# Kernel optimization log

Measured on AMD Instinct MI355X. Metric: run time of the kernel, lower is better.

Reference implementation:

```python
import jax, jax.numpy as jnp
import numpy as np

V, E, H, T, B = 10004, 96, 670, 20, 256


def setup_inputs() -> dict:
    key = jax.random.key(0)
    ks = iter(jax.random.split(key, 48))
    def p(*shape):
        return jax.random.normal(next(ks), shape, jnp.float32) * 0.05
    emb = p(V, E).at[0].set(0.0)  # padding_idx=0 row zeroed
    return dict(
        x=jax.random.randint(next(ks), (B, T), 0, V, jnp.int32),
        emb=emb,
        g_wi=p(4 * H, E), g_wh=p(4 * H, H), g_bi=p(4 * H), g_bh=p(4 * H),
        l_wi=p(4 * H, E), l_wh=p(4 * H, H), l_bi=p(4 * H), l_bh=p(4 * H),
        gl1_w=p(E, H), gl1_b=p(E), ll1_w=p(E, H), ll1_b=p(E),
        gl2_w=p(V, E), gl2_b=p(V), ll2_w=p(V, E), ll2_b=p(V),
        p1_w=p(500, E + 2 * H), p1_b=p(500),
        p2_w=p(250, 500), p2_b=p(250),
        p3_w=p(100, 250), p3_b=p(100),
        p4_w=p(50, 100), p4_b=p(50),
        pe_w=p(2, 50), pe_b=p(2),
        q1_w=p(75, 192), q1_b=p(75),
        q2_w=p(30, 75), q2_b=p(30),
        q2e_w=p(2, 30), q2e_b=p(2),
        q3_w=p(10, 30), q3_b=p(10),
        q3e_w=p(2, 10), q3e_b=p(2),
    )


def _lstm(x, h, c, wi, wh, bi, bh):
    # torch.nn.LSTMCell gate order: i, f, g, o
    g = x @ wi.T + bi + h @ wh.T + bh
    i, f, gg, o = jnp.split(g, 4, axis=-1)
    c = jax.nn.sigmoid(f) * c + jax.nn.sigmoid(i) * jnp.tanh(gg)
    h = jax.nn.sigmoid(o) * jnp.tanh(c)
    return h, c


def reference(x, emb, g_wi, g_wh, g_bi, g_bh, l_wi, l_wh, l_bi, l_bh,
              gl1_w, gl1_b, ll1_w, ll1_b, gl2_w, gl2_b, ll2_w, ll2_b,
              p1_w, p1_b, p2_w, p2_b, p3_w, p3_b, p4_w, p4_b, pe_w, pe_b,
              q1_w, q1_b, q2_w, q2_b, q2e_w, q2e_b, q3_w, q3_b, q3e_w, q3e_b):
    relu = jax.nn.relu
    embs = emb[x]                      # [B,T,E]
    Bb, Tt = x.shape
    Hh = g_wh.shape[1]
    z0 = jnp.zeros((Bb, Hh), embs.dtype)

    def step(carry, e_t):
        gh, gc, lh, lc = carry
        gh, gc = _lstm(e_t, gh, gc, g_wi, g_wh, g_bi, g_bh)
        lh, lc = _lstm(e_t, lh, lc, l_wi, l_wh, l_bi, l_bh)
        h = relu(jnp.concatenate([e_t, gh, lh], 1) @ p1_w.T + p1_b)
        h = relu(h @ p2_w.T + p2_b)
        h = relu(h @ p3_w.T + p3_b)
        h = relu(h @ p4_w.T + p4_b)
        prob = jax.nn.softmax(h @ pe_w.T + pe_b, axis=1)  # [B,2]
        # bmm([B,1,2],[B,2,H]) with tilde=[local, global]
        ghm = prob[:, 0:1] * lh + prob[:, 1:2] * gh
        gcm = prob[:, 0:1] * lc + prob[:, 1:2] * gc
        return (ghm, gcm, lh, lc), (ghm, prob)

    _, (hs, probs) = jax.lax.scan(step, (z0, z0, z0, z0), jnp.swapaxes(embs, 0, 1))
    hidden_states = jnp.swapaxes(hs, 0, 1)    # [B,T,H]
    probs_loop = jnp.swapaxes(probs, 0, 1)    # [B,T,2]

    global_x = hidden_states @ gl1_w.T + gl1_b  # [B,T,E]
    local_x = hidden_states @ ll1_w.T + ll1_b   # [B,T,E]
    sf = jnp.concatenate([global_x, local_x], -1)  # [B,T,192]
    h = relu(sf @ q1_w.T + q1_b)
    h = relu(h @ q2_w.T + q2_b)
    y = relu(h @ q2e_w.T + q2e_b)               # p1 logits [B,T,2]
    h2 = relu(h @ q3_w.T + q3_b)
    zz = relu(h2 @ q3e_w.T + q3e_b)             # p2 logits [B,T,2]

    p1s = jax.nn.softmax(y, axis=2)
    ph = jnp.broadcast_to(probs_loop[:, :, None, :], (Bb, Tt, Tt, 2))  # repeat(1,1,T,1)
    ph = jnp.concatenate([ph, p1s[:, None, :, :]], axis=1)
    xm = p1s[:, :, 0:1] * global_x + p1s[:, :, 1:2] * local_x
    gl = xm @ gl2_w.T + gl2_b                   # [B,T,V]
    ll = xm @ ll2_w.T + ll2_b
    p2s = jax.nn.softmax(zz, axis=2)
    ph = jnp.concatenate([ph, p2s[:, None, :, :]], axis=1)  # [B,T+2,T,2]
    logits = gl * p2s[:, :, 0:1] + ll * p2s[:, :, 1:2]
    return jnp.transpose(logits, (0, 2, 1)), ph
```

## Files before the change

kernel.cpp:

```cpp
#include <hip/hip_runtime.h>

#define DI __device__ __forceinline__

typedef unsigned short u16;
typedef unsigned int u32;
typedef __bf16 bf16x8 __attribute__((ext_vector_type(8)));
typedef float f32x4 __attribute__((ext_vector_type(4)));
typedef u32 u32x4 __attribute__((ext_vector_type(4)));

static constexpr int B = 256, Tn = 20, En = 96, Hn = 670, Vn = 10004;
static constexpr int HP = 672;
static constexpr int NBLK = 336;
static constexpr int GT = NBLK * 256;

DI float bf2f(u16 u) { union { u32 i; float f; } v; v.i = ((u32)u) << 16; return v.f; }
DI u16 f2bf(float f) {
    u32 u = __float_as_uint(f);
    u32 r = (u + 0x7FFFu + ((u >> 16) & 1u)) >> 16;
    return (u16)r;
}
DI float sigm(float x) { return 1.f / (1.f + __expf(-x)); }
DI float tanha(float x) {
    x = fminf(fmaxf(x, -15.f), 15.f);
    float e = __expf(2.f * x);
    return (e - 1.f) / (e + 1.f);
}
DI bf16x8 frag(const u16* p) { return *(const bf16x8*)p; }
DI f32x4 mfma16(bf16x8 a, bf16x8 b, f32x4 c) {
    return __builtin_amdgcn_mfma_f32_16x16x32_bf16(a, b, c, 0, 0, 0);
}
DI u16 ldw(const u16* src, long long i, int f) {
    return f ? f2bf(((const float*)src)[i]) : src[i];
}
DI float ldf(const u16* src, long long i, int f) {
    return f ? ((const float*)src)[i] : bf2f(src[i]);
}

DI u32x4 ldg16(const void* p) {
    u32x4 v;
    asm volatile("global_load_dwordx4 %0, %1, off sc0 sc1\n\ts_waitcnt vmcnt(0)"
                 : "=v"(v) : "v"(p));
    return v;
}
DI void ldg4f(const float* p0, const float* p1, const float* p2, const float* p3,
              float& a, float& b, float& c, float& d) {
    asm volatile("global_load_dword %0, %4, off sc0 sc1\n\t"
                 "global_load_dword %1, %5, off sc0 sc1\n\t"
                 "global_load_dword %2, %6, off sc0 sc1\n\t"
                 "global_load_dword %3, %7, off sc0 sc1\n\t"
                 "s_waitcnt vmcnt(0)"
                 : "=&v"(a), "=&v"(b), "=&v"(c), "=&v"(d)
                 : "v"(p0), "v"(p1), "v"(p2), "v"(p3));
}
DI u32 ldgu32(const u32* p) {
    u32 v;
    asm volatile("global_load_dword %0, %1, off sc0 sc1\n\ts_waitcnt vmcnt(0)"
                 : "=v"(v) : "v"(p));
    return v;
}
DI void stg32(float* p, float v) {
    asm volatile("global_store_dword %0, %1, off sc0 sc1" :: "v"(p), "v"(v) : "memory");
}
DI void stgu32(u32* p, u32 v) {
    asm volatile("global_store_dword %0, %1, off sc0 sc1" :: "v"(p), "v"(v) : "memory");
}
DI void stg16(u16* p, u16 v) {
    asm volatile("global_store_short %0, %1, off sc0 sc1" :: "v"(p), "v"((u32)v) : "memory");
}

struct Ptrs {
    const int* x;
    const u16 *emb, *g_wi, *g_wh, *g_bi, *g_bh, *l_wi, *l_wh, *l_bi, *l_bh;
    const u16 *gl1_w, *gl1_b, *ll1_w, *ll1_b, *gl2_w, *gl2_b, *ll2_w, *ll2_b;
    const u16 *p1_w, *p1_b, *p2_w, *p2_b, *p3_w, *p3_b, *p4_w, *p4_b, *pe_w, *pe_b;
    const u16 *q1_w, *q1_b, *q2_w, *q2_b, *q2e_w, *q2e_b, *q3_w, *q3_b, *q3e_w, *q3e_b;
    unsigned *bar;
    int  *flagp;
    u16 *embs;
    u16 *WgCat;
    u16 *P1W;
    u16 *W1C;
    u16 *W2C;
    float *BSUM;
    u16 *hs;
    u16 *hcat;
    u16 *uw;
    float *ghf, *gcf, *lhf, *lc2, *gcm;
    float *L1out;
    float *sf;
    float *p2sbuf;
    u16 *n_p1b, *n_p2w, *n_p2b, *n_p3w, *n_p3b, *n_p4w, *n_p4b, *n_pew, *n_peb;
    u16 *n_gl1b, *n_ll1b, *n_gl2b, *n_ll2b;
    u16 *n_q1w, *n_q1b, *n_q2w, *n_q2b, *n_q2ew, *n_q2eb, *n_q3w, *n_q3b, *n_q3ew, *n_q3eb;
    u16 *out0, *out1;
    float *out0f, *out1f;
};

template<bool HEAVY>
DI void gbar(unsigned* bar, int bid, int tid, unsigned gen) {
    __syncthreads();
    if (tid == 0) {
        if (HEAVY) __threadfence();
        else asm volatile("s_waitcnt vmcnt(0)" ::: "memory");
        stgu32(&bar[32 + bid * 16], gen);
    }
    if (bid == 0) {
        for (int i = tid; i < NBLK; i += 256) {
            while ((int)(ldgu32(&bar[32 + i * 16]) - gen) < 0)
                __builtin_amdgcn_s_sleep(4);
        }
        __syncthreads();
        if (tid == 0) stgu32(&bar[0], gen);
    } else if (tid == 0) {
        while ((int)(ldgu32(&bar[0]) - gen) < 0)
            __builtin_amdgcn_s_sleep(8);
    }
    __syncthreads();
    if (HEAVY) {
        if (tid == 0) __threadfence();
        __syncthreads();
    }
}

__global__ __launch_bounds__(256) void k_detect(Ptrs p) {
    int tid = threadIdx.x;
    for (int i = tid; i < 8192; i += 256) p.bar[i] = 0u;
    if (tid < 64) {
        u32 d = ((const u32*)p.g_bi)[tid];
        u16 lo = (u16)(d & 0xffffu);
        int e = (lo >> 7) & 0xff;
        unsigned long long m = __ballot(e >= 127);
        if (tid == 0) p.flagp[0] = (m != 0ull) ? 1 : 0;
    }
}

struct SMg { u16 Al[32 * 72]; u16 Wl[128 * 72]; float bs[128]; };
struct SMm { u16 Al[32 * 72]; u16 Wl[32 * 72]; };
struct SMr { float l1[500]; float h2s[250]; float h3s[100]; float h4s[52]; float pr[4]; };
struct SMs { u16 Al[64 * 40]; u16 Wl[64 * 40]; };
struct SMq {
    float sfl[3840];
    float h1[20][80]; float h2[20][32]; float h3[20][12];
    float yv[20][2]; float zv[20][2]; float p1s[20][2]; float p2sl[20][2];
};
union alignas(16) SMem { SMg g; SMm m; SMr r; SMs s; SMq q; };

DI void norm_phase(const Ptrs& p, int gtid, int f) {
    const u16* srcs[23] = {p.p1_b, p.p2_w, p.p2_b, p.p3_w, p.p3_b, p.p4_w, p.p4_b,
                           p.pe_w, p.pe_b, p.gl1_b, p.ll1_b, p.gl2_b, p.ll2_b,
                           p.q1_w, p.q1_b, p.q2_w, p.q2_b, p.q2e_w, p.q2e_b,
                           p.q3_w, p.q3_b, p.q3e_w, p.q3e_b};
    u16* dsts[23] = {p.n_p1b, p.n_p2w, p.n_p2b, p.n_p3w, p.n_p3b, p.n_p4w, p.n_p4b,
                     p.n_pew, p.n_peb, p.n_gl1b, p.n_ll1b, p.n_gl2b, p.n_ll2b,
                     p.n_q1w, p.n_q1b, p.n_q2w, p.n_q2b, p.n_q2ew, p.n_q2eb,
                     p.n_q3w, p.n_q3b, p.n_q3ew, p.n_q3eb};
    const int ns[23] = {500, 125000, 250, 25000, 100, 5000, 50, 100, 2, 96, 96, 10004, 10004,
                        14400, 75, 2250, 30, 60, 2, 300, 10, 20, 2};
    for (int i0 = gtid; i0 < 193351; i0 += GT) {
        int i = i0;
        #pragma unroll 1
        for (int s = 0; s < 23; ++s) {
            if (i < ns[s]) { dsts[s][i] = ldw(srcs[s], i, f); break; }
            i -= ns[s];
        }
    }
}

DI void prep_one(const Ptrs& p, int i, int f) {
    if (i < 491520) {
        int r = i / 96, j = i % 96;
        int t = r >> 8, b = r & 255;
        int idx = p.x[b * Tn + t];
        p.embs[r * 96 + j] = ldw(p.emb, (long long)idx * 96 + j, f);
        return;
    }
    i -= 491520;
    if (i < 2 * 2680 * 768) {
        int z = i / (2680 * 768);
        int rem = i - z * (2680 * 768);
        int col = rem / 768, k = rem % 768;
        const u16* wi = z ? p.l_wi : p.g_wi;
        const u16* wh = z ? p.l_wh : p.g_wh;
        u16 v = 0;
        if (k < 96) v = ldw(wi, col * 96 + k, f);
        else { int j = k - 96; if (j < 670) v = ldw(wh, col * 670 + j, f); }
        p.WgCat[i] = v;
        return;
    }
    i -= 2 * 2680 * 768;
    if (i < 512 * 1472) {
        int col = i / 1472, k = i % 1472;
        u16 v = 0;
        if (col < 500) {
            if (k < 96) v = ldw(p.p1_w, col * 1436 + k, f);
            else if (k < 768) { int j = k - 96;  if (j < 670) v = ldw(p.p1_w, col * 1436 + 96 + j, f); }
            else              { int j = k - 768; if (j < 670) v = ldw(p.p1_w, col * 1436 + 766 + j, f); }
        }
        p.P1W[i] = v;
        return;
    }
    i -= 512 * 1472;
    if (i < 192 * 672) {
        int o = i / 672, h = i % 672;
        u16 v = 0;
        if (h < 670) v = (o < 96) ? ldw(p.gl1_w, o * 670 + h, f) : ldw(p.ll1_w, (o - 96) * 670 + h, f);
        p.W1C[i] = v;
        return;
    }
    i -= 192 * 672;
    if (i < 10112 * 192) {
        int v_ = i / 192, k = i % 192;
        u16 v = 0;
        if (v_ < Vn) v = (k < 96) ? ldw(p.gl2_w, v_ * 96 + k, f) : ldw(p.ll2_w, v_ * 96 + (k - 96), f);
        p.W2C[i] = v;
        return;
    }
    i -= 10112 * 192;
    if (i < 2 * 2680) {
        int z = i / 2680, col = i % 2680;
        const u16* bi = z ? p.l_bi : p.g_bi;
        const u16* bh = z ? p.l_bh : p.g_bh;
        p.BSUM[i] = ldf(bi, col, f) + ldf(bh, col, f);
    }
}

DI void gates_tile(const Ptrs& p, int t, int tau, int tid, SMg& S) {
    const int z = tau / 168;
    const int rem = tau - z * 168;
    const int jt = rem % 21, mt = rem / 21;
    const int row0 = mt * 32, j0 = jt * 32;
    const int lane = tid & 63, wv = tid >> 6;

    __syncthreads();
    if (tid < 128) {
        int gate = tid >> 5, jj = tid & 31, j = j0 + jj;
        S.bs[tid] = (j < Hn) ? p.BSUM[z * 2680 + gate * Hn + j] : 0.f;
    }
    const int cur = t & 1, prv = cur ^ 1;
    f32x4 acc[4] = {};
    const int mtw = wv & 1, jh = wv >> 1;

    for (int kc = 0; kc < 12; ++kc) {
        const int kb = kc * 64;
        __syncthreads();
        #pragma unroll
        for (int it = 0; it < 4; ++it) {
            int idx = tid + it * 256;
            int ri = idx >> 3, k8 = (idx & 7) * 8;
            int gate = ri >> 5, jj = ri & 31, j = j0 + jj;
            u32x4 val = {0, 0, 0, 0};
            if (j < Hn) val = *(const u32x4*)&p.WgCat[(z * 2680 + gate * Hn + j) * 768 + kb + k8];
            *(u32x4*)&S.Wl[ri * 72 + k8] = val;
        }
        {
            int r = tid >> 3, k8 = (tid & 7) * 8, k = kb + k8;
            int b = row0 + r;
            u32x4 val = {0, 0, 0, 0};
            if (k < 96) val = *(const u32x4*)&p.embs[(t * 256 + b) * 96 + k];
            else if (t > 0) {
                int kk = k - 96;
                const u16* src = (z == 0) ? (p.hs + (b * Tn + (t - 1)) * HP + kk)
                                          : (p.hcat + prv * (B * 1344) + b * 1344 + 672 + kk);
                val = ldg16(src);
            }
            *(u32x4*)&S.Al[r * 72 + k8] = val;
        }
        __syncthreads();
        #pragma unroll
        for (int ks = 0; ks < 2; ++ks) {
            bf16x8 a = frag(&S.Al[(mtw * 16 + (lane & 15)) * 72 + ks * 32 + (lane >> 4) * 8]);
            #pragma unroll
            for (int g = 0; g < 4; ++g) {
                int nt = g * 2 + jh;
                bf16x8 bb = frag(&S.Wl[(nt * 16 + (lane & 15)) * 72 + ks * 32 + (lane >> 4) * 8]);
                acc[g] = mfma16(a, bb, acc[g]);
            }
        }
    }
    const int q = lane >> 4;
    const int jj = jh * 16 + (lane & 15);
    const int j = j0 + jj;
    const bool valid = (j < Hn);
    float cp0 = 0.f, cp1 = 0.f, cp2 = 0.f, cp3 = 0.f;
    const int b0 = row0 + mtw * 16 + q * 4;
    if (valid && t > 0) {
        const float* cb = (z == 0) ? (p.gcm + j) : (p.lc2 + prv * (B * Hn) + j);
        ldg4f(cb + (long long)(b0 + 0) * Hn, cb + (long long)(b0 + 1) * Hn,
              cb + (long long)(b0 + 2) * Hn, cb + (long long)(b0 + 3) * Hn,
              cp0, cp1, cp2, cp3);
    }
    float cps[4] = {cp0, cp1, cp2, cp3};
    #pragma unroll
    for (int r = 0; r < 4; ++r) {
        int b = b0 + r;
        float I = fminf(fmaxf(acc[0][r] + S.bs[jj], -30.f), 30.f);
        float F = fminf(fmaxf(acc[1][r] + S.bs[32 + jj], -30.f), 30.f);
        float G = fminf(fmaxf(acc[2][r] + S.bs[64 + jj], -30.f), 30.f);
        float O = fminf(fmaxf(acc[3][r] + S.bs[96 + jj], -30.f), 30.f);
        float c = sigm(F) * cps[r] + sigm(I) * tanha(G);
        float h = sigm(O) * tanha(c);
        if (z == 0) {
            if (valid) { stg32(&p.ghf[b * Hn + j], h); stg32(&p.gcf[b * Hn + j], c); }
            stg16(&p.hcat[cur * (B * 1344) + b * 1344 + j], valid ? f2bf(h) : (u16)0);
        } else {
            if (valid) { stg32(&p.lhf[b * Hn + j], h); stg32(&p.lc2[cur * (B * Hn) + b * Hn + j], c); }
            stg16(&p.hcat[cur * (B * 1344) + b * 1344 + 672 + j], valid ? f2bf(h) : (u16)0);
        }
    }
}

DI void mlp1_tile(const Ptrs& p, int t, int bid, int tid, SMm& S) {
    const int col0 = (bid & 15) * 32;
    const int row0 = (bid >> 4) * 32;
    const int lane = tid & 63, wv = tid >> 6;
    const int cur = t & 1;
    f32x4 acc = {};
    const int mtw = wv & 1, nh = wv >> 1;
    for (int kc = 0; kc < 23; ++kc) {
        const int kb = kc * 64;
        __syncthreads();
        {
            int ri = tid >> 3, k8 = (tid & 7) * 8;
            *(u32x4*)&S.Wl[ri * 72 + k8] = *(const u32x4*)&p.P1W[(col0 + ri) * 1472 + kb + k8];
        }
        {
            int r = tid >> 3, k8 = (tid & 7) * 8, k = kb + k8;
            int b = row0 + r;
            u32x4 val = {0, 0, 0, 0};
            if (k < 96) val = *(const u32x4*)&p.embs[(t * 256 + b) * 96 + k];
            else if (k < 1440) val = ldg16(&p.hcat[cur * (B * 1344) + b * 1344 + (k - 96)]);
            *(u32x4*)&S.Al[r * 72 + k8] = val;
        }
        __syncthreads();
        #pragma unroll
        for (int ks = 0; ks < 2; ++ks) {
            bf16x8 a = frag(&S.Al[(mtw * 16 + (lane & 15)) * 72 + ks * 32 + (lane >> 4) * 8]);
            bf16x8 bb = frag(&S.Wl[(nh * 16 + (lane & 15)) * 72 + ks * 32 + (lane >> 4) * 8]);
            acc = mfma16(a, bb, acc);
        }
    }
    const int q = lane >> 4;
    int col = col0 + nh * 16 + (lane & 15);
    if (col < 500) {
        float bias = bf2f(p.n_p1b[col]);
        #pragma unroll
        for (int r = 0; r < 4; ++r) {
            int b = row0 + mtw * 16 + q * 4 + r;
            stg32(&p.L1out[b * 500 + col], fmaxf(acc[r] + bias, 0.f));
        }
    }
}

DI void rest_block(const Ptrs& p, int t, int b, int tid, int f, SMr& S) {
    if (tid < 125) {
        u32x4 v = ldg16(&p.L1out[b * 500 + tid * 4]);
        *(u32x4*)&S.l1[tid * 4] = v;
    }
    __syncthreads();
    if (tid < 250) {
        const u16* wr = p.n_p2w + tid * 500;
        float s = 0.f;
        for (int k = 0; k < 500; k += 4) {
            uint2 u = *(const uint2*)&wr[k];
            s += S.l1[k]     * bf2f((u16)(u.x & 0xffff));
            s += S.l1[k + 1] * bf2f((u16)(u.x >> 16));
            s += S.l1[k + 2] * bf2f((u16)(u.y & 0xffff));
            s += S.l1[k + 3] * bf2f((u16)(u.y >> 16));
        }
        S.h2s[tid] = fmaxf(s + bf2f(p.n_p2b[tid]), 0.f);
    }
    __syncthreads();
    if (tid < 100) {
        const u16* wr = p.n_p3w + tid * 250;
        float s = 0.f;
        for (int k = 0; k < 250; k += 2) {
            u32 u = *(const u32*)&wr[k];
            s += S.h2s[k]     * bf2f((u16)(u & 0xffff));
            s += S.h2s[k + 1] * bf2f((u16)(u >> 16));
        }
        S.h3s[tid] = fmaxf(s + bf2f(p.n_p3b[tid]), 0.f);
    }
    __syncthreads();
    if (tid < 50) {
        const u16* wr = p.n_p4w + tid * 100;
        float s = 0.f;
        for (int k = 0; k < 100; k += 4) {
            uint2 u = *(const uint2*)&wr[k];
            s += S.h3s[k]     * bf2f((u16)(u.x & 0xffff));
            s += S.h3s[k + 1] * bf2f((u16)(u.x >> 16));
            s += S.h3s[k + 2] * bf2f((u16)(u.y & 0xffff));
            s += S.h3s[k + 3] * bf2f((u16)(u.y >> 16));
        }
        S.h4s[tid] = fmaxf(s + bf2f(p.n_p4b[tid]), 0.f);
    }
    __syncthreads();
    if (tid == 0) {
        float e0 = bf2f(p.n_peb[0]), e1 = bf2f(p.n_peb[1]);
        for (int k = 0; k < 50; ++k) {
            e0 += S.h4s[k] * bf2f(p.n_pew[k]);
            e1 += S.h4s[k] * bf2f(p.n_pew[50 + k]);
        }
        float m = fmaxf(e0, e1);
        float a0 = __expf(e0 - m), a1 = __expf(e1 - m);
        float inv = 1.f / (a0 + a1);
        S.pr[0] = a0 * inv; S.pr[1] = a1 * inv;
    }
    __syncthreads();
    float p0 = S.pr[0], p1 = S.pr[1];
    const int cur = t & 1;
    for (int j = tid; j < HP; j += 256) {
        u16 hv = 0;
        if (j < Hn) {
            float lh, gh, lc, gc;
            ldg4f(&p.lhf[b * Hn + j], &p.ghf[b * Hn + j],
                  &p.lc2[cur * (B * Hn) + b * Hn + j], &p.gcf[b * Hn + j], lh, gh, lc, gc);
            float gm = p0 * lh + p1 * gh;
            float cm = p0 * lc + p1 * gc;
            stg32(&p.gcm[b * Hn + j], cm);
            hv = f2bf(gm);
        }
        stg16(&p.hs[(b * Tn + t) * HP + j], hv);
    }
    if (tid < 40) {
        long long idx = b * 880 + t * 40 + tid;
        float v = (tid & 1) ? p1 : p0;
        if (f) p.out1f[idx] = v; else p.out1[idx] = f2bf(v);
    }
}

DI void sf_tile(const Ptrs& p, int tau, int tid, SMs& S) {
    const int col0 = (tau % 3) * 64;
    const int row0 = (tau / 3) * 64;
    const int lane = tid & 63, wv = tid >> 6;
    f32x4 acc[4] = {};
    for (int kc = 0; kc < 21; ++kc) {
        const int kb = kc * 32;
        __syncthreads();
        {
            int r = tid >> 2, k8 = (tid & 3) * 8;
            *(u32x4*)&S.Wl[r * 40 + k8] = *(const u32x4*)&p.W1C[(col0 + r) * HP + kb + k8];
            *(u32x4*)&S.Al[r * 40 + k8] = ldg16(&p.hs[(row0 + r) * HP + kb + k8]);
        }
        __syncthreads();
        bf16x8 a = frag(&S.Al[(wv * 16 + (lane & 15)) * 40 + (lane >> 4) * 8]);
        #pragma unroll
        for (int nt = 0; nt < 4; ++nt) {
            bf16x8 bb = frag(&S.Wl[(nt * 16 + (lane & 15)) * 40 + (lane >> 4) * 8]);
            acc[nt] = mfma16(a, bb, acc[nt]);
        }
    }
    const int q = lane >> 4;
    #pragma unroll
    for (int nt = 0; nt < 4; ++nt) {
        int col = col0 + nt * 16 + (lane & 15);
        float bias = bf2f(col < 96 ? p.n_gl1b[col] : p.n_ll1b[col - 96]);
        #pragma unroll
        for (int r = 0; r < 4; ++r) {
            int row = row0 + wv * 16 + q * 4 + r;
            stg32(&p.sf[row * 192 + col], acc[nt][r] + bias);
        }
    }
}

DI void qchain_block(const Ptrs& p, int b, int tid, int f, SMq& S) {
    for (int i = tid; i < 960; i += 256) {
        u32x4 v = ldg16(&p.sf[b * 3840 + i * 4]);
        *(u32x4*)&S.sfl[i * 4] = v;
    }
    __syncthreads();
    for (int u = tid; u < 1500; u += 256) {
        int row = u / 75, o = u % 75;
        const u16* wr = p.n_q1w + o * 192;
        const float* sr = &S.sfl[row * 192];
        float s = bf2f(p.n_q1b[o]);
        for (int k = 0; k < 192; k += 4) {
            uint2 w = *(const uint2*)&wr[k];
            s += sr[k]     * bf2f((u16)(w.x & 0xffff));
            s += sr[k + 1] * bf2f((u16)(w.x >> 16));
            s += sr[k + 2] * bf2f((u16)(w.y & 0xffff));
            s += sr[k + 3] * bf2f((u16)(w.y >> 16));
        }
        S.h1[row][o] = fmaxf(s, 0.f);
    }
    __syncthreads();
    for (int u = tid; u < 600; u += 256) {
        int row = u / 30, o = u % 30;
        const u16* wr = p.n_q2w + o * 75;
        float s = bf2f(p.n_q2b[o]);
        for (int k = 0; k < 75; ++k) s += S.h1[row][k] * bf2f(wr[k]);
        S.h2[row][o] = fmaxf(s, 0.f);
    }
    __syncthreads();
    if (tid < 40) {
        int row = tid >> 1, o = tid & 1;
        const u16* wr = p.n_q2ew + o * 30;
        float s = bf2f(p.n_q2eb[o]);
        for (int k = 0; k < 30; ++k) s += S.h2[row][k] * bf2f(wr[k]);
        S.yv[row][o] = fmaxf(s, 0.f);
    } else if (tid >= 56 && tid < 256) {
        int u = tid - 56;
        int row = u / 10, o = u % 10;
        const u16* wr = p.n_q3w + o * 30;
        float s = bf2f(p.n_q3b[o]);
        for (int k = 0; k < 30; ++k) s += S.h2[row][k] * bf2f(wr[k]);
        S.h3[row][o] = fmaxf(s, 0.f);
    }
    __syncthreads();
    if (tid < 40) {
        int row = tid >> 1, o = tid & 1;
        const u16* wr = p.n_q3ew + o * 10;
        float s = bf2f(p.n_q3eb[o]);
        for (int k = 0; k < 10; ++k) s += S.h3[row][k] * bf2f(wr[k]);
        S.zv[row][o] = fmaxf(s, 0.f);
    } else if (tid >= 64 && tid < 84) {
        int row = tid - 64;
        float m = fmaxf(S.yv[row][0], S.yv[row][1]);
        float a0 = __expf(S.yv[row][0] - m), a1 = __expf(S.yv[row][1] - m);
        float inv = 1.f / (a0 + a1);
        S.p1s[row][0] = a0 * inv; S.p1s[row][1] = a1 * inv;
    }
    __syncthreads();
    if (tid < 20) {
        float m = fmaxf(S.zv[tid][0], S.zv[tid][1]);
        float a0 = __expf(S.zv[tid][0] - m), a1 = __expf(S.zv[tid][1] - m);
        float inv = 1.f / (a0 + a1);
        S.p2sl[tid][0] = a0 * inv; S.p2sl[tid][1] = a1 * inv;
        p.p2sbuf[(b * Tn + tid) * 2]     = a0 * inv;
        p.p2sbuf[(b * Tn + tid) * 2 + 1] = a1 * inv;
    } else if (tid >= 64 && tid < 104) {
        int row = (tid - 64) >> 1, c = (tid - 64) & 1;
        long long idx = b * 880 + 800 + row * 2 + c;
        if (f) p.out1f[idx] = S.p1s[row][c]; else p.out1[idx] = f2bf(S.p1s[row][c]);
    }
    __syncthreads();
    for (int u = tid; u < 1920; u += 256) {
        int row = u / 96, e = u % 96;
        float xm = S.p1s[row][0] * S.sfl[row * 192 + e] + S.p1s[row][1] * S.sfl[row * 192 + 96 + e];
        p.uw[(b * Tn + row) * 192 + e]      = f2bf(S.p2sl[row][0] * xm);
        p.uw[(b * Tn + row) * 192 + 96 + e] = f2bf(S.p2sl[row][1] * xm);
    }
    if (tid < 40) {
        int row = tid >> 1, c = tid & 1;
        long long idx = b * 880 + 840 + row * 2 + c;
        if (f) p.out1f[idx] = S.p2sl[row][c]; else p.out1[idx] = f2bf(S.p2sl[row][c]);
    }
}

__global__ __launch_bounds__(256, 2) void k_loop(Ptrs p) {
    const int bid = blockIdx.x;
    const int tid = threadIdx.x;
    const int f = p.flagp[0];
    const int gtid = bid * 256 + tid;
    unsigned gen = 0;

    __shared__ SMem sm;

    norm_phase(p, gtid, f);
    #pragma unroll 1
    for (int i0 = gtid; i0 < 7437552; i0 += GT) prep_one(p, i0, f);
    gbar<true>(p.bar, bid, tid, ++gen);

    #pragma unroll 1
    for (int t = 0; t < Tn; ++t) {
        gates_tile(p, t, bid, tid, sm.g);
        gbar<false>(p.bar, bid, tid, ++gen);
        if (bid < 128) mlp1_tile(p, t, bid, tid, sm.m);
        gbar<false>(p.bar, bid, tid, ++gen);
        if (bid < 256) rest_block(p, t, bid, tid, f, sm.r);
        gbar<false>(p.bar, bid, tid, ++gen);
    }

    if (bid < 240) sf_tile(p, bid, tid, sm.s);
    gbar<false>(p.bar, bid, tid, ++gen);
    if (bid < 256) qchain_block(p, bid, tid, f, sm.q);
}

__global__ __launch_bounds__(256) void k_final(Ptrs p) {
    const int n0 = blockIdx.x * 64;
    const int v0 = blockIdx.y * 128;
    const int tid = threadIdx.x, lane = tid & 63, wv = tid >> 6;
    const int f = p.flagp[0];
    __shared__ u16 Wl[128 * 104];
    __shared__ u16 Ul[64 * 104];
    f32x4 acc[2][4] = {};
    const int m = lane & 15, q = lane >> 4;
    for (int kc = 0; kc < 2; ++kc) {
        const int kb = kc * 96;
        __syncthreads();
        for (int i = tid; i < 1536; i += 256) {
            int ri = i / 12, k8 = (i % 12) * 8;
            *(uint4*)&Wl[ri * 104 + k8] = *(const uint4*)&p.W2C[(v0 + ri) * 192 + kb + k8];
        }
        for (int i = tid; i < 768; i += 256) {
            int ri = i / 12, k8 = (i % 12) * 8;
            *(uint4*)&Ul[ri * 104 + k8] = *(const uint4*)&p.uw[(n0 + ri) * 192 + kb + k8];
        }
        __syncthreads();
        #pragma unroll
        for (int ks = 0; ks < 3; ++ks) {
            int ko = ks * 32 + q * 8;
            bf16x8 a0 = frag(&Wl[(wv * 32 + m) * 104 + ko]);
            bf16x8 a1 = frag(&Wl[(wv * 32 + 16 + m) * 104 + ko]);
            #pragma unroll
            for (int ni = 0; ni < 4; ++ni) {
                bf16x8 bb = frag(&Ul[(ni * 16 + m) * 104 + ko]);
                acc[0][ni] = mfma16(a0, bb, acc[0][ni]);
                acc[1][ni] = mfma16(a1, bb, acc[1][ni]);
            }
        }
    }
    #pragma unroll
    for (int ni = 0; ni < 4; ++ni) {
        int n = n0 + ni * 16 + m;
        int bb = n / 20, tt = n % 20;
        float s0 = p.p2sbuf[n * 2], s1 = p.p2sbuf[n * 2 + 1];
        size_t base = (size_t)bb * 200080 + tt;
        #pragma unroll
        for (int mi = 0; mi < 2; ++mi) {
            #pragma unroll
            for (int r = 0; r < 4; ++r) {
                int v = v0 + wv * 32 + mi * 16 + q * 4 + r;
                if (v < Vn) {
                    float val = acc[mi][ni][r] + s0 * bf2f(p.n_gl2b[v]) + s1 * bf2f(p.n_ll2b[v]);
                    size_t idx = base + (size_t)v * 20;
                    if (f) p.out0f[idx] = val; else p.out0[idx] = f2bf(val);
                }
            }
        }
    }
}

extern "C" void kernel_launch(void* const* d_in, const int* in_sizes, int n_in,
                              void* d_out, int out_size, void* d_ws, size_t ws_size,
                              hipStream_t stream) {
    Ptrs p;
    p.x    = (const int*)d_in[0];
    p.emb  = (const u16*)d_in[1];
    p.g_wi = (const u16*)d_in[2];  p.g_wh = (const u16*)d_in[3];
    p.g_bi = (const u16*)d_in[4];  p.g_bh = (const u16*)d_in[5];
    p.l_wi = (const u16*)d_in[6];  p.l_wh = (const u16*)d_in[7];
    p.l_bi = (const u16*)d_in[8];  p.l_bh = (const u16*)d_in[9];
    p.gl1_w = (const u16*)d_in[10]; p.gl1_b = (const u16*)d_in[11];
    p.ll1_w = (const u16*)d_in[12]; p.ll1_b = (const u16*)d_in[13];
    p.gl2_w = (const u16*)d_in[14]; p.gl2_b = (const u16*)d_in[15];
    p.ll2_w = (const u16*)d_in[16]; p.ll2_b = (const u16*)d_in[17];
    p.p1_w = (const u16*)d_in[18]; p.p1_b = (const u16*)d_in[19];
    p.p2_w = (const u16*)d_in[20]; p.p2_b = (const u16*)d_in[21];
    p.p3_w = (const u16*)d_in[22]; p.p3_b = (const u16*)d_in[23];
    p.p4_w = (const u16*)d_in[24]; p.p4_b = (const u16*)d_in[25];
    p.pe_w = (const u16*)d_in[26]; p.pe_b = (const u16*)d_in[27];
    p.q1_w = (const u16*)d_in[28]; p.q1_b = (const u16*)d_in[29];
    p.q2_w = (const u16*)d_in[30]; p.q2_b = (const u16*)d_in[31];
    p.q2e_w = (const u16*)d_in[32]; p.q2e_b = (const u16*)d_in[33];
    p.q3_w = (const u16*)d_in[34]; p.q3_b = (const u16*)d_in[35];
    p.q3e_w = (const u16*)d_in[36]; p.q3e_b = (const u16*)d_in[37];

    char* w = (char*)d_ws;
    auto carve = [&](size_t bytes) { char* r = w; w += (bytes + 255) & ~(size_t)255; return r; };
    p.bar    = (unsigned*)carve(32768);
    p.flagp  = (int*)carve(256);
    p.embs   = (u16*)carve((size_t)20 * 256 * 96 * 2);
    p.WgCat  = (u16*)carve((size_t)2 * 2680 * 768 * 2);
    p.P1W    = (u16*)carve((size_t)512 * 1472 * 2);
    p.W1C    = (u16*)carve((size_t)192 * 672 * 2);
    p.W2C    = (u16*)carve((size_t)10112 * 192 * 2);
    p.BSUM   = (float*)carve((size_t)2 * 2680 * 4);
    p.hs     = (u16*)carve((size_t)5120 * 672 * 2);
    p.hcat   = (u16*)carve((size_t)2 * 256 * 1344 * 2);
    p.uw     = (u16*)carve((size_t)5120 * 192 * 2);
    p.ghf    = (float*)carve((size_t)256 * 670 * 4);
    p.gcf    = (float*)carve((size_t)256 * 670 * 4);
    p.lhf    = (float*)carve((size_t)256 * 670 * 4);
    p.lc2    = (float*)carve((size_t)2 * 256 * 670 * 4);
    p.gcm    = (float*)carve((size_t)256 * 670 * 4);
    p.L1out  = (float*)carve((size_t)256 * 500 * 4);
    p.sf     = (float*)carve((size_t)5120 * 192 * 4);
    p.p2sbuf = (float*)carve((size_t)5120 * 2 * 4);
    p.n_p1b = (u16*)carve(500 * 2);   p.n_p2w = (u16*)carve(125000 * 2);
    p.n_p2b = (u16*)carve(250 * 2);   p.n_p3w = (u16*)carve(25000 * 2);
    p.n_p3b = (u16*)carve(100 * 2);   p.n_p4w = (u16*)carve(5000 * 2);
    p.n_p4b = (u16*)carve(50 * 2);    p.n_pew = (u16*)carve(100 * 2);
    p.n_peb = (u16*)carve(2 * 2);
    p.n_gl1b = (u16*)carve(96 * 2);   p.n_ll1b = (u16*)carve(96 * 2);
    p.n_gl2b = (u16*)carve(10004 * 2); p.n_ll2b = (u16*)carve(10004 * 2);
    p.n_q1w = (u16*)carve(14400 * 2); p.n_q1b = (u16*)carve(75 * 2);
    p.n_q2w = (u16*)carve(2250 * 2);  p.n_q2b = (u16*)carve(30 * 2);
    p.n_q2ew = (u16*)carve(60 * 2);   p.n_q2eb = (u16*)carve(2 * 2);
    p.n_q3w = (u16*)carve(300 * 2);   p.n_q3b = (u16*)carve(10 * 2);
    p.n_q3ew = (u16*)carve(20 * 2);   p.n_q3eb = (u16*)carve(2 * 2);
    p.out0 = (u16*)d_out;
    p.out1 = p.out0 + 51220480;
    p.out0f = (float*)d_out;
    p.out1f = p.out0f + 51220480;

    k_detect<<<1, 256, 0, stream>>>(p);
    k_loop<<<NBLK, 256, 0, stream>>>(p);
    k_final<<<dim3(80, 79), 256, 0, stream>>>(p);
}
```

Measured before the change: 1.956 ms.

## Use per-timestep state buffers with cached loads and remap gate tiles to blocks

Replaces the double-buffered recurrent state (hcat, lc2, gcm, hs) with a separate buffer per timestep. Because each step now writes a fresh address, reads can use ordinary cached vector loads instead of the special coherent ldg16/ldg4f loads. The hs layout becomes time-major, so the sf tile computes a remapped row pointer. The grid grows to 384 blocks, and gate tiles get a new mapping from block index to (z, jt, mt), with some blocks idle. The cost is a larger workspace footprint and more blocks taking part in every grid barrier.

```diff
diff --git a/kernel.cpp b/kernel.cpp
--- a/kernel.cpp
+++ b/kernel.cpp
@@ -10,7 +10,7 @@
 
 static constexpr int B = 256, Tn = 20, En = 96, Hn = 670, Vn = 10004;
 static constexpr int HP = 672;
-static constexpr int NBLK = 336;
+static constexpr int NBLK = 384;
 static constexpr int GT = NBLK * 256;
 
 DI float bf2f(u16 u) { union { u32 i; float f; } v; v.i = ((u32)u) << 16; return v.f; }
@@ -85,7 +85,9 @@
     u16 *hs;
     u16 *hcat;
     u16 *uw;
-    float *ghf, *gcf, *lhf, *lc2, *gcm;
+    float *ghf, *gcf, *lhf;
+    float *lc2;
+    float *gcm;
     float *L1out;
     float *sf;
     float *p2sbuf;
@@ -224,10 +226,7 @@
     }
 }
 
-DI void gates_tile(const Ptrs& p, int t, int tau, int tid, SMg& S) {
-    const int z = tau / 168;
-    const int rem = tau - z * 168;
-    const int jt = rem % 21, mt = rem / 21;
+DI void gates_tile(const Ptrs& p, int t, int z, int jt, int mt, int tid, SMg& S) {
     const int row0 = mt * 32, j0 = jt * 32;
     const int lane = tid & 63, wv = tid >> 6;
 
@@ -236,7 +235,6 @@
         int gate = tid >> 5, jj = tid & 31, j = j0 + jj;
         S.bs[tid] = (j < Hn) ? p.BSUM[z * 2680 + gate * Hn + j] : 0.f;
     }
-    const int cur = t & 1, prv = cur ^ 1;
     f32x4 acc[4] = {};
     const int mtw = wv & 1, jh = wv >> 1;
 
@@ -259,9 +257,9 @@
             if (k < 96) val = *(const u32x4*)&p.embs[(t * 256 + b) * 96 + k];
             else if (t > 0) {
                 int kk = k - 96;
-                const u16* src = (z == 0) ? (p.hs + (b * Tn + (t - 1)) * HP + kk)
-                                          : (p.hcat + prv * (B * 1344) + b * 1344 + 672 + kk);
-                val = ldg16(src);
+                const u16* src = (z == 0) ? (p.hs + ((t - 1) * B + b) * HP + kk)
+                                          : (p.hcat + (t - 1) * (B * 1344) + b * 1344 + 672 + kk);
+                val = *(const u32x4*)src;
             }
             *(u32x4*)&S.Al[r * 72 + k8] = val;
         }
@@ -281,15 +279,13 @@
     const int jj = jh * 16 + (lane & 15);
     const int j = j0 + jj;
     const bool valid = (j < Hn);
-    float cp0 = 0.f, cp1 = 0.f, cp2 = 0.f, cp3 = 0.f;
     const int b0 = row0 + mtw * 16 + q * 4;
+    float cps[4] = {0.f, 0.f, 0.f, 0.f};
     if (valid && t > 0) {
-        const float* cb = (z == 0) ? (p.gcm + j) : (p.lc2 + prv * (B * Hn) + j);
-        ldg4f(cb + (long long)(b0 + 0) * Hn, cb + (long long)(b0 + 1) * Hn,
-              cb + (long long)(b0 + 2) * Hn, cb + (long long)(b0 + 3) * Hn,
-              cp0, cp1, cp2, cp3);
-    }
-    float cps[4] = {cp0, cp1, cp2, cp3};
+        const float* cb = ((z == 0) ? p.gcm : p.lc2) + (t - 1) * (B * Hn) + j;
+        #pragma unroll
+        for (int r = 0; r < 4; ++r) cps[r] = cb[(b0 + r) * Hn];
+    }
     #pragma unroll
     for (int r = 0; r < 4; ++r) {
         int b = b0 + r;
@@ -301,10 +297,10 @@
         float h = sigm(O) * tanha(c);
         if (z == 0) {
             if (valid) { stg32(&p.ghf[b * Hn + j], h); stg32(&p.gcf[b * Hn + j], c); }
-            stg16(&p.hcat[cur * (B * 1344) + b * 1344 + j], valid ? f2bf(h) : (u16)0);
+            stg16(&p.hcat[t * (B * 1344) + b * 1344 + j], valid ? f2bf(h) : (u16)0);
         } else {
-            if (valid) { stg32(&p.lhf[b * Hn + j], h); stg32(&p.lc2[cur * (B * Hn) + b * Hn + j], c); }
-            stg16(&p.hcat[cur * (B * 1344) + b * 1344 + 672 + j], valid ? f2bf(h) : (u16)0);
+            if (valid) { stg32(&p.lhf[b * Hn + j], h); stg32(&p.lc2[t * (B * Hn) + b * Hn + j], c); }
+            stg16(&p.hcat[t * (B * 1344) + b * 1344 + 672 + j], valid ? f2bf(h) : (u16)0);
         }
     }
 }
@@ -313,7 +309,6 @@
     const int col0 = (bid & 15) * 32;
     const int row0 = (bid >> 4) * 32;
     const int lane = tid & 63, wv = tid >> 6;
-    const int cur = t & 1;
     f32x4 acc = {};
     const int mtw = wv & 1, nh = wv >> 1;
     for (int kc = 0; kc < 23; ++kc) {
@@ -328,7 +323,7 @@
             int b = row0 + r;
             u32x4 val = {0, 0, 0, 0};
             if (k < 96) val = *(const u32x4*)&p.embs[(t * 256 + b) * 96 + k];
-            else if (k < 1440) val = ldg16(&p.hcat[cur * (B * 1344) + b * 1344 + (k - 96)]);
+            else if (k < 1440) val = *(const u32x4*)&p.hcat[t * (B * 1344) + b * 1344 + (k - 96)];
             *(u32x4*)&S.Al[r * 72 + k8] = val;
         }
         __syncthreads();
@@ -407,19 +402,18 @@
     }
     __syncthreads();
     float p0 = S.pr[0], p1 = S.pr[1];
-    const int cur = t & 1;
     for (int j = tid; j < HP; j += 256) {
         u16 hv = 0;
         if (j < Hn) {
             float lh, gh, lc, gc;
             ldg4f(&p.lhf[b * Hn + j], &p.ghf[b * Hn + j],
-                  &p.lc2[cur * (B * Hn) + b * Hn + j], &p.gcf[b * Hn + j], lh, gh, lc, gc);
+                  &p.lc2[t * (B * Hn) + b * Hn + j], &p.gcf[b * Hn + j], lh, gh, lc, gc);
             float gm = p0 * lh + p1 * gh;
             float cm = p0 * lc + p1 * gc;
-            stg32(&p.gcm[b * Hn + j], cm);
+            stg32(&p.gcm[t * (B * Hn) + b * Hn + j], cm);
             hv = f2bf(gm);
         }
-        stg16(&p.hs[(b * Tn + t) * HP + j], hv);
+        stg16(&p.hs[(t * B + b) * HP + j], hv);
     }
     if (tid < 40) {
         long long idx = b * 880 + t * 40 + tid;
@@ -432,6 +426,8 @@
     const int col0 = (tau % 3) * 64;
     const int row0 = (tau / 3) * 64;
     const int lane = tid & 63, wv = tid >> 6;
+    const int n = row0 + (tid >> 2);
+    const u16* arow = p.hs + ((n % Tn) * B + (n / Tn)) * HP;
     f32x4 acc[4] = {};
     for (int kc = 0; kc < 21; ++kc) {
         const int kb = kc * 32;
@@ -439,7 +435,7 @@
         {
             int r = tid >> 2, k8 = (tid & 3) * 8;
             *(u32x4*)&S.Wl[r * 40 + k8] = *(const u32x4*)&p.W1C[(col0 + r) * HP + kb + k8];
-            *(u32x4*)&S.Al[r * 40 + k8] = ldg16(&p.hs[(row0 + r) * HP + kb + k8]);
+            *(u32x4*)&S.Al[r * 40 + k8] = *(const u32x4*)&arow[kb + k8];
         }
         __syncthreads();
         bf16x8 a = frag(&S.Al[(wv * 16 + (lane & 15)) * 40 + (lane >> 4) * 8]);
@@ -463,10 +459,8 @@
 }
 
 DI void qchain_block(const Ptrs& p, int b, int tid, int f, SMq& S) {
-    for (int i = tid; i < 960; i += 256) {
-        u32x4 v = ldg16(&p.sf[b * 3840 + i * 4]);
-        *(u32x4*)&S.sfl[i * 4] = v;
-    }
+    for (int i = tid; i < 960; i += 256)
+        *(float4*)&S.sfl[i * 4] = *(const float4*)&p.sf[b * 3840 + i * 4];
     __syncthreads();
     for (int u = tid; u < 1500; u += 256) {
         int row = u / 75, o = u % 75;
@@ -560,9 +554,13 @@
     for (int i0 = gtid; i0 < 7437552; i0 += GT) prep_one(p, i0, f);
     gbar<true>(p.bar, bid, tid, ++gen);
 
+    const int gx = bid & 7, gg = bid >> 3;
+    const int gz = gx >> 2, gjt = (gx & 3) * 6 + (gg >> 3), gmt = gg & 7;
+    const bool gvalid = (gjt < 21);
+
     #pragma unroll 1
     for (int t = 0; t < Tn; ++t) {
-        gates_tile(p, t, bid, tid, sm.g);
+        if (gvalid) gates_tile(p, t, gz, gjt, gmt, tid, sm.g);
         gbar<false>(p.bar, bid, tid, ++gen);
         if (bid < 128) mlp1_tile(p, t, bid, tid, sm.m);
         gbar<false>(p.bar, bid, tid, ++gen);
@@ -665,14 +663,14 @@
     p.W1C    = (u16*)carve((size_t)192 * 672 * 2);
     p.W2C    = (u16*)carve((size_t)10112 * 192 * 2);
     p.BSUM   = (float*)carve((size_t)2 * 2680 * 4);
-    p.hs     = (u16*)carve((size_t)5120 * 672 * 2);
-    p.hcat   = (u16*)carve((size_t)2 * 256 * 1344 * 2);
+    p.hs     = (u16*)carve((size_t)20 * 256 * 672 * 2);
+    p.hcat   = (u16*)carve((size_t)20 * 256 * 1344 * 2);
     p.uw     = (u16*)carve((size_t)5120 * 192 * 2);
     p.ghf    = (float*)carve((size_t)256 * 670 * 4);
     p.gcf    = (float*)carve((size_t)256 * 670 * 4);
     p.lhf    = (float*)carve((size_t)256 * 670 * 4);
-    p.lc2    = (float*)carve((size_t)2 * 256 * 670 * 4);
-    p.gcm    = (float*)carve((size_t)256 * 670 * 4);
+    p.lc2    = (float*)carve((size_t)20 * 256 * 670 * 4);
+    p.gcm    = (float*)carve((size_t)20 * 256 * 670 * 4);
     p.L1out  = (float*)carve((size_t)256 * 500 * 4);
     p.sf     = (float*)carve((size_t)5120 * 192 * 4);
     p.p2sbuf = (float*)carve((size_t)5120 * 2 * 4);
```

Result: faster. 1.840 ms (-5.9%).
